# Kernel tuning notes

Hardware: AMD Instinct MI355X
Metric: run time of the kernel (lower is better)

The kernel has to match this reference:

```python
import jax, jax.numpy as jnp
import numpy as np

N = 50000          # nodes
E = 625000         # edges
H = 128            # hidden_dim
L = 4              # num_layers
G = 2000           # number of graphs in batch
NODE_F = 9
EDGE_F = 4
LN_EPS = 1e-5


def setup_inputs() -> dict:
    key = jax.random.key(0)
    ks = jax.random.split(key, 14)
    s = 0.05
    return {
        "x": jax.random.normal(ks[0], (N, NODE_F), jnp.float32),
        "edge_index": jax.random.randint(ks[1], (2, E), 0, N, dtype=jnp.int32),
        "edge_attr": jax.random.normal(ks[2], (E, EDGE_F), jnp.float32),
        "batch": jnp.sort(jax.random.randint(ks[3], (N,), 0, G, dtype=jnp.int32)),
        # node / edge encoders
        "Wn": jax.random.normal(ks[4], (NODE_F, H), jnp.float32) * s,
        "bn": jnp.zeros((H,), jnp.float32),
        "We": jax.random.normal(ks[5], (EDGE_F, H), jnp.float32) * s,
        "be": jnp.zeros((H,), jnp.float32),
        # per-layer GINE MLP params (stacked over layers)
        "W1": jax.random.normal(ks[6], (L, H, 2 * H), jnp.float32) * s,
        "b1": jnp.zeros((L, 2 * H), jnp.float32),
        "W2": jax.random.normal(ks[7], (L, 2 * H, H), jnp.float32) * s,
        "b2": jnp.zeros((L, H), jnp.float32),
        # per-layer LayerNorm params
        "gamma": jnp.ones((L, H), jnp.float32),
        "beta": jnp.zeros((L, H), jnp.float32),
    }


def reference(x, edge_index, edge_attr, batch, Wn, bn, We, be, W1, b1, W2, b2, gamma, beta):
    h = x @ Wn + bn                       # [N, H]
    ea = edge_attr @ We + be              # [E, H]
    src, dst = edge_index[0], edge_index[1]
    for l in range(L):
        res = h
        # GINEConv (eps=0): out = mlp(x + sum_j relu(x_j + e_ij))
        msg = jax.nn.relu(h[src] + ea)                              # [E, H] gather+add+relu
        agg = jax.ops.segment_sum(msg, dst, num_segments=N)        # scatter-sum -> [N, H]
        z = h + agg
        z = jax.nn.relu(z @ W1[l] + b1[l]) @ W2[l] + b2[l]          # 2-layer MLP
        mu = jnp.mean(z, axis=-1, keepdims=True)
        var = jnp.mean((z - mu) ** 2, axis=-1, keepdims=True)
        z = (z - mu) * jax.lax.rsqrt(var + LN_EPS) * gamma[l] + beta[l]
        h = jax.nn.relu(z) + res                                    # relu + residual
    # global_add_pool
    return jax.ops.segment_sum(h, batch, num_segments=G)            # [G, H]
```

## Files before the change

### kernel.cpp

```cpp
#include <hip/hip_runtime.h>

typedef unsigned short ushort_t;
typedef __attribute__((ext_vector_type(8))) __bf16 bf16x8;
typedef __attribute__((ext_vector_type(4))) float f32x4;

#define HD 128
#define NL 4
#define SCAN_C 2048

__device__ __forceinline__ ushort_t f2bf(float f){
  unsigned u = __builtin_bit_cast(unsigned, f);
  unsigned r = (u + 0x7FFFu + ((u >> 16) & 1u)) >> 16;
  return (ushort_t)r;
}

__device__ __forceinline__ float bf2f(ushort_t u){
  unsigned v = ((unsigned)u) << 16;
  return __builtin_bit_cast(float, v);
}

__device__ __forceinline__ f32x4 mfma16(bf16x8 a, bf16x8 b, f32x4 c){
  return __builtin_amdgcn_mfma_f32_16x16x32_bf16(a, b, c, 0, 0, 0);
}

__global__ void hist_kernel(const int* __restrict__ dst, int* __restrict__ deg, int E){
  int e = blockIdx.x * 256 + threadIdx.x;
  if (e < E) atomicAdd(&deg[dst[e]], 1);
}

__global__ void ghist_kernel(const int* __restrict__ batch, int* __restrict__ gdeg, int N){
  int n = blockIdx.x * 256 + threadIdx.x;
  if (n < N) atomicAdd(&gdeg[batch[n]], 1);
}

__global__ void scan_part(const int* __restrict__ in, int* __restrict__ bsum, int n){
  int b = blockIdx.x, tid = threadIdx.x;
  int base = b * SCAN_C + tid * 8;
  int s = 0;
  if (base + 8 <= n){
    int4 a = *(const int4*)(in + base);
    int4 c = *(const int4*)(in + base + 4);
    s = a.x + a.y + a.z + a.w + c.x + c.y + c.z + c.w;
  } else {
    #pragma unroll
    for (int k = 0; k < 8; ++k) if (base + k < n) s += in[base + k];
  }
  #pragma unroll
  for (int o = 1; o < 64; o <<= 1) s += __shfl_xor(s, o, 64);
  __shared__ int ws[4];
  int lane = tid & 63, wid = tid >> 6;
  if (lane == 0) ws[wid] = s;
  __syncthreads();
  if (tid == 0) bsum[b] = ws[0] + ws[1] + ws[2] + ws[3];
}

__global__ void scan_top(const int* __restrict__ bsum, int* __restrict__ bofs,
                         int* __restrict__ outn, int B){
  int tid = threadIdx.x;
  int v = (tid < B) ? bsum[tid] : 0;
  int lane = tid & 63, wid = tid >> 6;
  int inc = v;
  #pragma unroll
  for (int o = 1; o < 64; o <<= 1){
    int t = __shfl_up(inc, o, 64);
    if (lane >= o) inc += t;
  }
  __shared__ int ws[4];
  if (lane == 63) ws[wid] = inc;
  __syncthreads();
  int wprev = 0;
  for (int i = 0; i < wid; ++i) wprev += ws[i];
  if (tid < B) bofs[tid] = inc - v + wprev;
  if (tid == 0) *outn = ws[0] + ws[1] + ws[2] + ws[3];
}

__global__ void scan_final(const int* __restrict__ in, const int* __restrict__ bofs,
                           int* __restrict__ out, int* __restrict__ cur, int n){
  int b = blockIdx.x, tid = threadIdx.x;
  int base = b * SCAN_C + tid * 8;
  int v[8];
  if (base + 8 <= n){
    *(int4*)(v)     = *(const int4*)(in + base);
    *(int4*)(v + 4) = *(const int4*)(in + base + 4);
  } else {
    #pragma unroll
    for (int k = 0; k < 8; ++k) v[k] = (base + k < n) ? in[base + k] : 0;
  }
  int tsum = 0;
  #pragma unroll
  for (int k = 0; k < 8; ++k) tsum += v[k];
  int lane = tid & 63, wid = tid >> 6;
  int inc = tsum;
  #pragma unroll
  for (int o = 1; o < 64; o <<= 1){
    int t = __shfl_up(inc, o, 64);
    if (lane >= o) inc += t;
  }
  __shared__ int ws[4];
  if (lane == 63) ws[wid] = inc;
  __syncthreads();
  int run = bofs[b] + inc - tsum;
  for (int i = 0; i < wid; ++i) run += ws[i];
  #pragma unroll
  for (int k = 0; k < 8; ++k){
    int i = base + k;
    if (i < n){
      out[i] = run;
      if (cur) cur[i] = run;
      run += v[k];
    }
  }
}

__global__ void scatter_kernel(const int* __restrict__ src, const int* __restrict__ dst,
                               const float4* __restrict__ ea, int* __restrict__ cursor,
                               int* __restrict__ srcs_s, float4* __restrict__ ea4_s, int E){
  int e = blockIdx.x * 256 + threadIdx.x;
  if (e < E){
    int d = dst[e];
    int p = atomicAdd(&cursor[d], 1);
    srcs_s[p] = src[e];
    ea4_s[p] = ea[e];
  }
}

__global__ void wconv_kernel(const float* __restrict__ W1, const float* __restrict__ W2,
                             ushort_t* __restrict__ W1t, ushort_t* __restrict__ W2t){
  int i = blockIdx.x * 256 + threadIdx.x;
  if (i < NL * 32768){
    int l = i >> 15, r = i & 32767;
    int n = r >> 7, k = r & 127;
    W1t[i] = f2bf(W1[l * 32768 + k * 256 + n]);
  } else {
    int i2 = i - NL * 32768;
    int l = i2 >> 15, r = i2 & 32767;
    int n = r >> 8, k = r & 255;
    W2t[i2] = f2bf(W2[l * 32768 + k * 128 + n]);
  }
}

__global__ void encoder_kernel(const float* __restrict__ x, const float* __restrict__ Wn,
                               const float* __restrict__ bn, float* __restrict__ h,
                               ushort_t* __restrict__ hb, int N){
  int n = blockIdx.x, j = threadIdx.x;
  float acc = bn[j];
  #pragma unroll
  for (int k = 0; k < 9; ++k) acc = fmaf(x[n * 9 + k], Wn[k * HD + j], acc);
  h[(size_t)n * HD + j] = acc;
  hb[(size_t)n * HD + j] = f2bf(acc);
}

__global__ void agg_kernel(const float* __restrict__ h, const ushort_t* __restrict__ hb,
                           const int* __restrict__ off, const int* __restrict__ srcs,
                           const float4* __restrict__ ea4, const float* __restrict__ We,
                           const float* __restrict__ be, ushort_t* __restrict__ z, int N){
  int n = blockIdx.x, j = threadIdx.x;
  float w0 = We[j], w1 = We[HD + j], w2 = We[2 * HD + j], w3 = We[3 * HD + j];
  float bj = be[j];
  int s = off[n], e = off[n + 1];
  float acc = h[(size_t)n * HD + j];
  int i = s;
  for (; i + 4 <= e; i += 4){
    int s0 = srcs[i], s1 = srcs[i + 1], s2 = srcs[i + 2], s3 = srcs[i + 3];
    float4 a0 = ea4[i], a1 = ea4[i + 1], a2 = ea4[i + 2], a3 = ea4[i + 3];
    float h0 = bf2f(hb[(size_t)s0 * HD + j]);
    float h1 = bf2f(hb[(size_t)s1 * HD + j]);
    float h2 = bf2f(hb[(size_t)s2 * HD + j]);
    float h3 = bf2f(hb[(size_t)s3 * HD + j]);
    float e0 = fmaf(a0.x, w0, fmaf(a0.y, w1, fmaf(a0.z, w2, fmaf(a0.w, w3, bj))));
    float e1 = fmaf(a1.x, w0, fmaf(a1.y, w1, fmaf(a1.z, w2, fmaf(a1.w, w3, bj))));
    float e2 = fmaf(a2.x, w0, fmaf(a2.y, w1, fmaf(a2.z, w2, fmaf(a2.w, w3, bj))));
    float e3 = fmaf(a3.x, w0, fmaf(a3.y, w1, fmaf(a3.z, w2, fmaf(a3.w, w3, bj))));
    acc += fmaxf(h0 + e0, 0.f);
    acc += fmaxf(h1 + e1, 0.f);
    acc += fmaxf(h2 + e2, 0.f);
    acc += fmaxf(h3 + e3, 0.f);
  }
  for (; i < e; ++i){
    int sc = srcs[i];
    float4 a = ea4[i];
    float eav = fmaf(a.x, w0, fmaf(a.y, w1, fmaf(a.z, w2, fmaf(a.w, w3, bj))));
    acc += fmaxf(bf2f(hb[(size_t)sc * HD + j]) + eav, 0.f);
  }
  z[(size_t)n * HD + j] = f2bf(acc);
}

__global__ __launch_bounds__(256, 2) void mlp1_kernel(
    const ushort_t* __restrict__ z, const ushort_t* __restrict__ Bt,
    const float* __restrict__ bias, ushort_t* __restrict__ outp, int N){
  extern __shared__ char smem[];
  char* As = smem;
  char* Bs = smem + 32768;
  int tid = threadIdx.x;
  int r0 = blockIdx.x * 128;
  int c0 = blockIdx.y * 128;
  #pragma unroll
  for (int i = 0; i < 8; ++i){
    int g = i * 256 + tid;
    int row = g >> 4, kg = g & 15;
    int lb = row * 256 + ((kg * 16) ^ ((row & 7) << 4));
    int ar = min(r0 + row, N - 1);
    *(bf16x8*)(As + lb) = *(const bf16x8*)(z + (size_t)ar * 128 + kg * 8);
    *(bf16x8*)(Bs + lb) = *(const bf16x8*)(Bt + (size_t)(c0 + row) * 128 + kg * 8);
  }
  __syncthreads();
  int w = tid >> 6, l = tid & 63;
  int wr = w >> 1, wc = w & 1;
  int lr = l & 15, lk = l >> 4;
  f32x4 acc[4][4] = {};
  #pragma unroll
  for (int ks = 0; ks < 4; ++ks){
    int kb = ks * 64 + lk * 16;
    bf16x8 a[4], b[4];
    #pragma unroll
    for (int fm = 0; fm < 4; ++fm){
      int row = wr * 64 + fm * 16 + lr;
      a[fm] = *(const bf16x8*)(As + row * 256 + (kb ^ ((row & 7) << 4)));
    }
    #pragma unroll
    for (int fn = 0; fn < 4; ++fn){
      int col = wc * 64 + fn * 16 + lr;
      b[fn] = *(const bf16x8*)(Bs + col * 256 + (kb ^ ((col & 7) << 4)));
    }
    #pragma unroll
    for (int fm = 0; fm < 4; ++fm)
      #pragma unroll
      for (int fn = 0; fn < 4; ++fn)
        acc[fm][fn] = mfma16(a[fm], b[fn], acc[fm][fn]);
  }
  float bv[4];
  #pragma unroll
  for (int fn = 0; fn < 4; ++fn) bv[fn] = bias[c0 + wc * 64 + fn * 16 + lr];
  #pragma unroll
  for (int fm = 0; fm < 4; ++fm){
    #pragma unroll
    for (int r = 0; r < 4; ++r){
      int row = r0 + wr * 64 + fm * 16 + lk * 4 + r;
      if (row < N){
        #pragma unroll
        for (int fn = 0; fn < 4; ++fn){
          int col = c0 + wc * 64 + fn * 16 + lr;
          outp[(size_t)row * 256 + col] = f2bf(fmaxf(acc[fm][fn][r] + bv[fn], 0.f));
        }
      }
    }
  }
}

__global__ __launch_bounds__(256, 2) void mlp2_kernel(
    const ushort_t* __restrict__ tin, const ushort_t* __restrict__ Bt,
    const float* __restrict__ b2, const float* __restrict__ gamma,
    const float* __restrict__ beta, float* __restrict__ h,
    ushort_t* __restrict__ hb, int N){
  extern __shared__ char smem[];
  char* As = smem;
  char* Bs = smem + 32768;
  float* z2 = (float*)smem;
  float* stat = (float*)(smem + 66560);
  int tid = threadIdx.x;
  int r0 = blockIdx.x * 128;
  int w = tid >> 6, l = tid & 63;
  int wr = w >> 1, wc = w & 1;
  int lr = l & 15, lk = l >> 4;
  f32x4 acc[4][4] = {};
  for (int kh = 0; kh < 2; ++kh){
    #pragma unroll
    for (int i = 0; i < 8; ++i){
      int g = i * 256 + tid;
      int row = g >> 4, kg = g & 15;
      int lb = row * 256 + ((kg * 16) ^ ((row & 7) << 4));
      int ar = min(r0 + row, N - 1);
      *(bf16x8*)(As + lb) = *(const bf16x8*)(tin + (size_t)ar * 256 + kh * 128 + kg * 8);
      *(bf16x8*)(Bs + lb) = *(const bf16x8*)(Bt + (size_t)row * 256 + kh * 128 + kg * 8);
    }
    __syncthreads();
    #pragma unroll
    for (int ks = 0; ks < 4; ++ks){
      int kb = ks * 64 + lk * 16;
      bf16x8 a[4], b[4];
      #pragma unroll
      for (int fm = 0; fm < 4; ++fm){
        int row = wr * 64 + fm * 16 + lr;
        a[fm] = *(const bf16x8*)(As + row * 256 + (kb ^ ((row & 7) << 4)));
      }
      #pragma unroll
      for (int fn = 0; fn < 4; ++fn){
        int col = wc * 64 + fn * 16 + lr;
        b[fn] = *(const bf16x8*)(Bs + col * 256 + (kb ^ ((col & 7) << 4)));
      }
      #pragma unroll
      for (int fm = 0; fm < 4; ++fm)
        #pragma unroll
        for (int fn = 0; fn < 4; ++fn)
          acc[fm][fn] = mfma16(a[fm], b[fn], acc[fm][fn]);
    }
    __syncthreads();
  }
  float bv[4];
  #pragma unroll
  for (int fn = 0; fn < 4; ++fn) bv[fn] = b2[wc * 64 + fn * 16 + lr];
  #pragma unroll
  for (int fm = 0; fm < 4; ++fm)
    #pragma unroll
    for (int r = 0; r < 4; ++r){
      int row = wr * 64 + fm * 16 + lk * 4 + r;
      #pragma unroll
      for (int fn = 0; fn < 4; ++fn){
        int col = wc * 64 + fn * 16 + lr;
        z2[row * 130 + col] = acc[fm][fn][r] + bv[fn];
      }
    }
  __syncthreads();
  {
    int row = tid >> 1, hf = tid & 1;
    const float* q = z2 + row * 130 + hf * 64;
    float s = 0.f, qq = 0.f;
    #pragma unroll
    for (int i = 0; i < 32; ++i){
      float2 v = *(const float2*)(q + i * 2);
      s += v.x + v.y; qq += v.x * v.x + v.y * v.y;
    }
    s += __shfl_xor(s, 1, 64);
    qq += __shfl_xor(qq, 1, 64);
    if (hf == 0){
      float mean = s * (1.f / 128.f);
      float var = qq * (1.f / 128.f) - mean * mean;
      stat[row] = mean;
      stat[128 + row] = rsqrtf(var + 1e-5f);
    }
  }
  __syncthreads();
  #pragma unroll 4
  for (int it = 0; it < 32; ++it){
    int row = it * 4 + (tid >> 6);
    int grow = r0 + row;
    if (grow < N){
      int col = (tid & 63) * 2;
      float2 v = *(const float2*)(z2 + row * 130 + col);
      float m = stat[row], rs = stat[128 + row];
      float2 g = *(const float2*)(gamma + col);
      float2 bt = *(const float2*)(beta + col);
      float2 hr = *(const float2*)(h + (size_t)grow * HD + col);
      float2 ov;
      ov.x = fmaxf((v.x - m) * rs * g.x + bt.x, 0.f) + hr.x;
      ov.y = fmaxf((v.y - m) * rs * g.y + bt.y, 0.f) + hr.y;
      *(float2*)(h + (size_t)grow * HD + col) = ov;
      ushort_t b0 = f2bf(ov.x), b1v = f2bf(ov.y);
      *(unsigned*)(hb + (size_t)grow * HD + col) = (unsigned)b0 | ((unsigned)b1v << 16);
    }
  }
}

__global__ void pool_kernel(const float* __restrict__ h, const int* __restrict__ goff,
                            float* __restrict__ outp, int G){
  int g = blockIdx.x, j = threadIdx.x;
  int s = goff[g], e = goff[g + 1];
  float acc = 0.f;
  for (int i = s; i < e; ++i) acc += h[(size_t)i * HD + j];
  outp[(size_t)g * HD + j] = acc;
}

extern "C" void kernel_launch(void* const* d_in, const int* in_sizes, int n_in,
                              void* d_out, int out_size, void* d_ws, size_t ws_size,
                              hipStream_t stream){
  const float* x     = (const float*)d_in[0];
  const int*   ei    = (const int*)  d_in[1];
  const float* eattr = (const float*)d_in[2];
  const int*   batch = (const int*)  d_in[3];
  const float* Wn    = (const float*)d_in[4];
  const float* bn    = (const float*)d_in[5];
  const float* We    = (const float*)d_in[6];
  const float* be    = (const float*)d_in[7];
  const float* W1    = (const float*)d_in[8];
  const float* b1    = (const float*)d_in[9];
  const float* W2    = (const float*)d_in[10];
  const float* b2    = (const float*)d_in[11];
  const float* gamma = (const float*)d_in[12];
  const float* beta  = (const float*)d_in[13];
  float* outp = (float*)d_out;

  int N = in_sizes[3];
  int E = in_sizes[2] / 4;
  int G = out_size / HD;

  char* base = (char*)d_ws;
  size_t o = 0;
  auto alloc = [&](size_t bytes)->char*{
    char* r = base + o; o = (o + bytes + 255) & ~(size_t)255; return r;
  };
  float*    h    = (float*)   alloc((size_t)N * HD * 4);
  ushort_t* hb   = (ushort_t*)alloc((size_t)N * HD * 2);
  ushort_t* z    = (ushort_t*)alloc((size_t)N * HD * 2);
  ushort_t* t    = (ushort_t*)alloc((size_t)N * 2 * HD * 2);
  ushort_t* W1t  = (ushort_t*)alloc((size_t)NL * 2 * HD * HD * 2);
  ushort_t* W2t  = (ushort_t*)alloc((size_t)NL * 2 * HD * HD * 2);
  int* deg    = (int*)alloc((size_t)N * 4);
  int* gdeg   = (int*)alloc((size_t)G * 4);
  int* off    = (int*)alloc((size_t)(N + 1) * 4);
  int* goff   = (int*)alloc((size_t)(G + 1) * 4);
  int* cursor = (int*)alloc((size_t)N * 4);
  int* bsumN  = (int*)alloc(512 * 4);
  int* bofsN  = (int*)alloc(512 * 4);
  int* bsumG  = (int*)alloc(512 * 4);
  int* bofsG  = (int*)alloc(512 * 4);
  int* srcs_s = (int*)alloc((size_t)E * 4);
  float4* ea4 = (float4*)alloc((size_t)E * 16);
  (void)ws_size; (void)n_in;

  const int* src = ei;
  const int* dst = ei + E;

  hipMemsetAsync(deg, 0, (size_t)N * 4, stream);
  hipMemsetAsync(gdeg, 0, (size_t)G * 4, stream);

  hist_kernel<<<(E + 255) / 256, 256, 0, stream>>>(dst, deg, E);
  ghist_kernel<<<(N + 255) / 256, 256, 0, stream>>>(batch, gdeg, N);

  int BN = (N + SCAN_C - 1) / SCAN_C;
  int BG = (G + SCAN_C - 1) / SCAN_C;
  scan_part<<<BN, 256, 0, stream>>>(deg, bsumN, N);
  scan_top<<<1, 256, 0, stream>>>(bsumN, bofsN, off + N, BN);
  scan_final<<<BN, 256, 0, stream>>>(deg, bofsN, off, cursor, N);
  scan_part<<<BG, 256, 0, stream>>>(gdeg, bsumG, G);
  scan_top<<<1, 256, 0, stream>>>(bsumG, bofsG, goff + G, BG);
  scan_final<<<BG, 256, 0, stream>>>(gdeg, bofsG, goff, (int*)nullptr, G);

  scatter_kernel<<<(E + 255) / 256, 256, 0, stream>>>(src, dst, (const float4*)eattr,
                                                      cursor, srcs_s, ea4, E);
  wconv_kernel<<<(2 * NL * 32768) / 256, 256, 0, stream>>>(W1, W2, W1t, W2t);
  encoder_kernel<<<N, HD, 0, stream>>>(x, Wn, bn, h, hb, N);

  int mblocks = (N + 127) / 128;
  for (int l = 0; l < NL; ++l){
    agg_kernel<<<N, HD, 0, stream>>>(h, hb, off, srcs_s, ea4, We, be, z, N);
    mlp1_kernel<<<dim3(mblocks, 2), 256, 65536, stream>>>(
        z, W1t + (size_t)l * 2 * HD * HD, b1 + l * 2 * HD, t, N);
    mlp2_kernel<<<mblocks, 256, 67584, stream>>>(
        t, W2t + (size_t)l * 2 * HD * HD, b2 + l * HD, gamma + l * HD, beta + l * HD, h, hb, N);
  }
  pool_kernel<<<G, HD, 0, stream>>>(h, goff, outp, G);
}
```

Measured before the change: 447.0 us.

## Fuse GINE MLP layers into one kernel and index edge attrs indirectly

```diff
diff --git a/kernel.cpp b/kernel.cpp
--- a/kernel.cpp
+++ b/kernel.cpp
@@ -113,14 +113,12 @@
 }
 
 __global__ void scatter_kernel(const int* __restrict__ src, const int* __restrict__ dst,
-                               const float4* __restrict__ ea, int* __restrict__ cursor,
-                               int* __restrict__ srcs_s, float4* __restrict__ ea4_s, int E){
+                               int* __restrict__ cursor, int2* __restrict__ se, int E){
   int e = blockIdx.x * 256 + threadIdx.x;
   if (e < E){
     int d = dst[e];
     int p = atomicAdd(&cursor[d], 1);
-    srcs_s[p] = src[e];
-    ea4_s[p] = ea[e];
+    se[p] = make_int2(src[e], e);
   }
 }
 
@@ -151,7 +149,7 @@
 }
 
 __global__ void agg_kernel(const float* __restrict__ h, const ushort_t* __restrict__ hb,
-                           const int* __restrict__ off, const int* __restrict__ srcs,
+                           const int* __restrict__ off, const int2* __restrict__ se,
                            const float4* __restrict__ ea4, const float* __restrict__ We,
                            const float* __restrict__ be, ushort_t* __restrict__ z, int N){
   int n = blockIdx.x, j = threadIdx.x;
@@ -161,12 +159,12 @@
   float acc = h[(size_t)n * HD + j];
   int i = s;
   for (; i + 4 <= e; i += 4){
-    int s0 = srcs[i], s1 = srcs[i + 1], s2 = srcs[i + 2], s3 = srcs[i + 3];
-    float4 a0 = ea4[i], a1 = ea4[i + 1], a2 = ea4[i + 2], a3 = ea4[i + 3];
-    float h0 = bf2f(hb[(size_t)s0 * HD + j]);
-    float h1 = bf2f(hb[(size_t)s1 * HD + j]);
-    float h2 = bf2f(hb[(size_t)s2 * HD + j]);
-    float h3 = bf2f(hb[(size_t)s3 * HD + j]);
+    int2 p0 = se[i], p1 = se[i + 1], p2 = se[i + 2], p3 = se[i + 3];
+    float4 a0 = ea4[p0.y], a1 = ea4[p1.y], a2 = ea4[p2.y], a3 = ea4[p3.y];
+    float h0 = bf2f(hb[(size_t)p0.x * HD + j]);
+    float h1 = bf2f(hb[(size_t)p1.x * HD + j]);
+    float h2 = bf2f(hb[(size_t)p2.x * HD + j]);
+    float h3 = bf2f(hb[(size_t)p3.x * HD + j]);
     float e0 = fmaf(a0.x, w0, fmaf(a0.y, w1, fmaf(a0.z, w2, fmaf(a0.w, w3, bj))));
     float e1 = fmaf(a1.x, w0, fmaf(a1.y, w1, fmaf(a1.z, w2, fmaf(a1.w, w3, bj))));
     float e2 = fmaf(a2.x, w0, fmaf(a2.y, w1, fmaf(a2.z, w2, fmaf(a2.w, w3, bj))));
@@ -177,176 +175,152 @@
     acc += fmaxf(h3 + e3, 0.f);
   }
   for (; i < e; ++i){
-    int sc = srcs[i];
-    float4 a = ea4[i];
+    int2 p = se[i];
+    float4 a = ea4[p.y];
     float eav = fmaf(a.x, w0, fmaf(a.y, w1, fmaf(a.z, w2, fmaf(a.w, w3, bj))));
-    acc += fmaxf(bf2f(hb[(size_t)sc * HD + j]) + eav, 0.f);
+    acc += fmaxf(bf2f(hb[(size_t)p.x * HD + j]) + eav, 0.f);
   }
   z[(size_t)n * HD + j] = f2bf(acc);
 }
 
-__global__ __launch_bounds__(256, 2) void mlp1_kernel(
-    const ushort_t* __restrict__ z, const ushort_t* __restrict__ Bt,
-    const float* __restrict__ bias, ushort_t* __restrict__ outp, int N){
-  extern __shared__ char smem[];
-  char* As = smem;
-  char* Bs = smem + 32768;
+__global__ __launch_bounds__(512, 4) void mlp_fused_kernel(
+    const ushort_t* __restrict__ zin, const ushort_t* __restrict__ W1t,
+    const float* __restrict__ b1, const ushort_t* __restrict__ W2t,
+    const float* __restrict__ b2, const float* __restrict__ gamma,
+    const float* __restrict__ beta, float* __restrict__ h,
+    ushort_t* __restrict__ hb, int N){
+  extern __shared__ char lds[];
   int tid = threadIdx.x;
   int r0 = blockIdx.x * 128;
-  int c0 = blockIdx.y * 128;
-  #pragma unroll
-  for (int i = 0; i < 8; ++i){
-    int g = i * 256 + tid;
+  #pragma unroll
+  for (int i = 0; i < 4; ++i){
+    int g = i * 512 + tid;
     int row = g >> 4, kg = g & 15;
     int lb = row * 256 + ((kg * 16) ^ ((row & 7) << 4));
     int ar = min(r0 + row, N - 1);
-    *(bf16x8*)(As + lb) = *(const bf16x8*)(z + (size_t)ar * 128 + kg * 8);
-    *(bf16x8*)(Bs + lb) = *(const bf16x8*)(Bt + (size_t)(c0 + row) * 128 + kg * 8);
-  }
-  __syncthreads();
+    *(bf16x8*)(lds + lb) = *(const bf16x8*)(zin + (size_t)ar * 128 + kg * 8);
+  }
   int w = tid >> 6, l = tid & 63;
-  int wr = w >> 1, wc = w & 1;
   int lr = l & 15, lk = l >> 4;
-  f32x4 acc[4][4] = {};
-  #pragma unroll
-  for (int ks = 0; ks < 4; ++ks){
-    int kb = ks * 64 + lk * 16;
-    bf16x8 a[4], b[4];
-    #pragma unroll
-    for (int fm = 0; fm < 4; ++fm){
-      int row = wr * 64 + fm * 16 + lr;
-      a[fm] = *(const bf16x8*)(As + row * 256 + (kb ^ ((row & 7) << 4)));
-    }
-    #pragma unroll
-    for (int fn = 0; fn < 4; ++fn){
-      int col = wc * 64 + fn * 16 + lr;
-      b[fn] = *(const bf16x8*)(Bs + col * 256 + (kb ^ ((col & 7) << 4)));
-    }
-    #pragma unroll
-    for (int fm = 0; fm < 4; ++fm)
-      #pragma unroll
-      for (int fn = 0; fn < 4; ++fn)
-        acc[fm][fn] = mfma16(a[fm], b[fn], acc[fm][fn]);
-  }
-  float bv[4];
-  #pragma unroll
-  for (int fn = 0; fn < 4; ++fn) bv[fn] = bias[c0 + wc * 64 + fn * 16 + lr];
-  #pragma unroll
-  for (int fm = 0; fm < 4; ++fm){
-    #pragma unroll
-    for (int r = 0; r < 4; ++r){
-      int row = r0 + wr * 64 + fm * 16 + lk * 4 + r;
-      if (row < N){
-        #pragma unroll
-        for (int fn = 0; fn < 4; ++fn){
-          int col = c0 + wc * 64 + fn * 16 + lr;
-          outp[(size_t)row * 256 + col] = f2bf(fmaxf(acc[fm][fn][r] + bv[fn], 0.f));
-        }
-      }
-    }
-  }
-}
-
-__global__ __launch_bounds__(256, 2) void mlp2_kernel(
-    const ushort_t* __restrict__ tin, const ushort_t* __restrict__ Bt,
-    const float* __restrict__ b2, const float* __restrict__ gamma,
-    const float* __restrict__ beta, float* __restrict__ h,
-    ushort_t* __restrict__ hb, int N){
-  extern __shared__ char smem[];
-  char* As = smem;
-  char* Bs = smem + 32768;
-  float* z2 = (float*)smem;
-  float* stat = (float*)(smem + 66560);
-  int tid = threadIdx.x;
-  int r0 = blockIdx.x * 128;
-  int w = tid >> 6, l = tid & 63;
-  int wr = w >> 1, wc = w & 1;
-  int lr = l & 15, lk = l >> 4;
-  f32x4 acc[4][4] = {};
-  for (int kh = 0; kh < 2; ++kh){
-    #pragma unroll
-    for (int i = 0; i < 8; ++i){
-      int g = i * 256 + tid;
-      int row = g >> 4, kg = g & 15;
-      int lb = row * 256 + ((kg * 16) ^ ((row & 7) << 4));
-      int ar = min(r0 + row, N - 1);
-      *(bf16x8*)(As + lb) = *(const bf16x8*)(tin + (size_t)ar * 256 + kh * 128 + kg * 8);
-      *(bf16x8*)(Bs + lb) = *(const bf16x8*)(Bt + (size_t)row * 256 + kh * 128 + kg * 8);
-    }
-    __syncthreads();
+  __syncthreads();
+  {
+    int wk = w >> 1, wn = w & 1;
+    f32x4 acc1[4][4] = {};
     #pragma unroll
     for (int ks = 0; ks < 4; ++ks){
       int kb = ks * 64 + lk * 16;
       bf16x8 a[4], b[4];
       #pragma unroll
       for (int fm = 0; fm < 4; ++fm){
-        int row = wr * 64 + fm * 16 + lr;
-        a[fm] = *(const bf16x8*)(As + row * 256 + (kb ^ ((row & 7) << 4)));
+        int k2r = wk * 64 + fm * 16 + lr;
+        a[fm] = *(const bf16x8*)((const char*)W1t + (size_t)k2r * 256 + kb);
       }
       #pragma unroll
       for (int fn = 0; fn < 4; ++fn){
-        int col = wc * 64 + fn * 16 + lr;
-        b[fn] = *(const bf16x8*)(Bs + col * 256 + (kb ^ ((col & 7) << 4)));
+        int node = wn * 64 + fn * 16 + lr;
+        b[fn] = *(const bf16x8*)(lds + node * 256 + (kb ^ ((node & 7) << 4)));
       }
       #pragma unroll
       for (int fm = 0; fm < 4; ++fm)
         #pragma unroll
         for (int fn = 0; fn < 4; ++fn)
-          acc[fm][fn] = mfma16(a[fm], b[fn], acc[fm][fn]);
+          acc1[fm][fn] = mfma16(a[fm], b[fn], acc1[fm][fn]);
     }
     __syncthreads();
-  }
-  float bv[4];
-  #pragma unroll
-  for (int fn = 0; fn < 4; ++fn) bv[fn] = b2[wc * 64 + fn * 16 + lr];
-  #pragma unroll
-  for (int fm = 0; fm < 4; ++fm)
-    #pragma unroll
-    for (int r = 0; r < 4; ++r){
-      int row = wr * 64 + fm * 16 + lk * 4 + r;
+    #pragma unroll
+    for (int fm = 0; fm < 4; ++fm){
+      f32x4 bv = *(const f32x4*)(b1 + wk * 64 + fm * 16 + lk * 4);
+      int k2b = (wk * 64 + fm * 16 + lk * 4) * 2;
       #pragma unroll
       for (int fn = 0; fn < 4; ++fn){
-        int col = wc * 64 + fn * 16 + lr;
-        z2[row * 130 + col] = acc[fm][fn][r] + bv[fn];
+        int node = wn * 64 + fn * 16 + lr;
+        ushort4 tv;
+        tv.x = f2bf(fmaxf(acc1[fm][fn][0] + bv[0], 0.f));
+        tv.y = f2bf(fmaxf(acc1[fm][fn][1] + bv[1], 0.f));
+        tv.z = f2bf(fmaxf(acc1[fm][fn][2] + bv[2], 0.f));
+        tv.w = f2bf(fmaxf(acc1[fm][fn][3] + bv[3], 0.f));
+        *(ushort4*)(lds + node * 512 + (k2b ^ ((node & 7) << 4))) = tv;
       }
     }
-  __syncthreads();
-  {
-    int row = tid >> 1, hf = tid & 1;
-    const float* q = z2 + row * 130 + hf * 64;
-    float s = 0.f, qq = 0.f;
-    #pragma unroll
-    for (int i = 0; i < 32; ++i){
-      float2 v = *(const float2*)(q + i * 2);
-      s += v.x + v.y; qq += v.x * v.x + v.y * v.y;
-    }
-    s += __shfl_xor(s, 1, 64);
-    qq += __shfl_xor(qq, 1, 64);
-    if (hf == 0){
-      float mean = s * (1.f / 128.f);
-      float var = qq * (1.f / 128.f) - mean * mean;
-      stat[row] = mean;
-      stat[128 + row] = rsqrtf(var + 1e-5f);
-    }
-  }
-  __syncthreads();
-  #pragma unroll 4
-  for (int it = 0; it < 32; ++it){
-    int row = it * 4 + (tid >> 6);
-    int grow = r0 + row;
-    if (grow < N){
-      int col = (tid & 63) * 2;
-      float2 v = *(const float2*)(z2 + row * 130 + col);
-      float m = stat[row], rs = stat[128 + row];
-      float2 g = *(const float2*)(gamma + col);
-      float2 bt = *(const float2*)(beta + col);
-      float2 hr = *(const float2*)(h + (size_t)grow * HD + col);
-      float2 ov;
-      ov.x = fmaxf((v.x - m) * rs * g.x + bt.x, 0.f) + hr.x;
-      ov.y = fmaxf((v.y - m) * rs * g.y + bt.y, 0.f) + hr.y;
-      *(float2*)(h + (size_t)grow * HD + col) = ov;
-      ushort_t b0 = f2bf(ov.x), b1v = f2bf(ov.y);
-      *(unsigned*)(hb + (size_t)grow * HD + col) = (unsigned)b0 | ((unsigned)b1v << 16);
+  }
+  __syncthreads();
+  int wd = w >> 1, wn2 = w & 1;
+  f32x4 acc2[2][4] = {};
+  #pragma unroll
+  for (int ks = 0; ks < 8; ++ks){
+    int kb = ks * 64 + lk * 16;
+    bf16x8 a2[2], bt2[4];
+    #pragma unroll
+    for (int fm = 0; fm < 2; ++fm){
+      int d = wd * 32 + fm * 16 + lr;
+      a2[fm] = *(const bf16x8*)((const char*)W2t + (size_t)d * 512 + kb);
+    }
+    #pragma unroll
+    for (int fn = 0; fn < 4; ++fn){
+      int node = wn2 * 64 + fn * 16 + lr;
+      bt2[fn] = *(const bf16x8*)(lds + node * 512 + (kb ^ ((node & 7) << 4)));
+    }
+    #pragma unroll
+    for (int fm = 0; fm < 2; ++fm)
+      #pragma unroll
+      for (int fn = 0; fn < 4; ++fn)
+        acc2[fm][fn] = mfma16(a2[fm], bt2[fn], acc2[fm][fn]);
+  }
+  __syncthreads();
+  float* stat_s = (float*)lds;
+  float* stat_q = (float*)(lds + 2048);
+  f32x4 b2v[2], gv[2], btv[2];
+  #pragma unroll
+  for (int fm = 0; fm < 2; ++fm){
+    int db = wd * 32 + fm * 16 + lk * 4;
+    b2v[fm] = *(const f32x4*)(b2 + db);
+    gv[fm]  = *(const f32x4*)(gamma + db);
+    btv[fm] = *(const f32x4*)(beta + db);
+  }
+  #pragma unroll
+  for (int fn = 0; fn < 4; ++fn){
+    float ss = 0.f, qq = 0.f;
+    #pragma unroll
+    for (int fm = 0; fm < 2; ++fm)
+      #pragma unroll
+      for (int r = 0; r < 4; ++r){
+        float v = acc2[fm][fn][r] + b2v[fm][r];
+        acc2[fm][fn][r] = v;
+        ss += v; qq += v * v;
+      }
+    ss += __shfl_xor(ss, 16, 64); ss += __shfl_xor(ss, 32, 64);
+    qq += __shfl_xor(qq, 16, 64); qq += __shfl_xor(qq, 32, 64);
+    if (l < 16){
+      int node = wn2 * 64 + fn * 16 + lr;
+      stat_s[node * 4 + wd] = ss;
+      stat_q[node * 4 + wd] = qq;
+    }
+  }
+  __syncthreads();
+  #pragma unroll
+  for (int fn = 0; fn < 4; ++fn){
+    int node = wn2 * 64 + fn * 16 + lr;
+    int gn = r0 + node;
+    float ss = stat_s[node * 4 + 0] + stat_s[node * 4 + 1] +
+               stat_s[node * 4 + 2] + stat_s[node * 4 + 3];
+    float qq = stat_q[node * 4 + 0] + stat_q[node * 4 + 1] +
+               stat_q[node * 4 + 2] + stat_q[node * 4 + 3];
+    float mean = ss * (1.f / 128.f);
+    float rs = rsqrtf(qq * (1.f / 128.f) - mean * mean + 1e-5f);
+    if (gn < N){
+      #pragma unroll
+      for (int fm = 0; fm < 2; ++fm){
+        int db = wd * 32 + fm * 16 + lk * 4;
+        f32x4 hold = *(const f32x4*)(h + (size_t)gn * HD + db);
+        f32x4 ov;
+        #pragma unroll
+        for (int r = 0; r < 4; ++r)
+          ov[r] = fmaxf((acc2[fm][fn][r] - mean) * rs * gv[fm][r] + btv[fm][r], 0.f) + hold[r];
+        *(f32x4*)(h + (size_t)gn * HD + db) = ov;
+        ushort4 hv;
+        hv.x = f2bf(ov[0]); hv.y = f2bf(ov[1]); hv.z = f2bf(ov[2]); hv.w = f2bf(ov[3]);
+        *(ushort4*)(hb + (size_t)gn * HD + db) = hv;
+      }
     }
   }
 }
@@ -391,7 +365,6 @@
   float*    h    = (float*)   alloc((size_t)N * HD * 4);
   ushort_t* hb   = (ushort_t*)alloc((size_t)N * HD * 2);
   ushort_t* z    = (ushort_t*)alloc((size_t)N * HD * 2);
-  ushort_t* t    = (ushort_t*)alloc((size_t)N * 2 * HD * 2);
   ushort_t* W1t  = (ushort_t*)alloc((size_t)NL * 2 * HD * HD * 2);
   ushort_t* W2t  = (ushort_t*)alloc((size_t)NL * 2 * HD * HD * 2);
   int* deg    = (int*)alloc((size_t)N * 4);
@@ -403,8 +376,7 @@
   int* bofsN  = (int*)alloc(512 * 4);
   int* bsumG  = (int*)alloc(512 * 4);
   int* bofsG  = (int*)alloc(512 * 4);
-  int* srcs_s = (int*)alloc((size_t)E * 4);
-  float4* ea4 = (float4*)alloc((size_t)E * 16);
+  int2* se    = (int2*)alloc((size_t)E * 8);
   (void)ws_size; (void)n_in;
 
   const int* src = ei;
@@ -425,18 +397,17 @@
   scan_top<<<1, 256, 0, stream>>>(bsumG, bofsG, goff + G, BG);
   scan_final<<<BG, 256, 0, stream>>>(gdeg, bofsG, goff, (int*)nullptr, G);
 
-  scatter_kernel<<<(E + 255) / 256, 256, 0, stream>>>(src, dst, (const float4*)eattr,
-                                                      cursor, srcs_s, ea4, E);
+  scatter_kernel<<<(E + 255) / 256, 256, 0, stream>>>(src, dst, cursor, se, E);
   wconv_kernel<<<(2 * NL * 32768) / 256, 256, 0, stream>>>(W1, W2, W1t, W2t);
   encoder_kernel<<<N, HD, 0, stream>>>(x, Wn, bn, h, hb, N);
 
   int mblocks = (N + 127) / 128;
   for (int l = 0; l < NL; ++l){
-    agg_kernel<<<N, HD, 0, stream>>>(h, hb, off, srcs_s, ea4, We, be, z, N);
-    mlp1_kernel<<<dim3(mblocks, 2), 256, 65536, stream>>>(
-        z, W1t + (size_t)l * 2 * HD * HD, b1 + l * 2 * HD, t, N);
-    mlp2_kernel<<<mblocks, 256, 67584, stream>>>(
-        t, W2t + (size_t)l * 2 * HD * HD, b2 + l * HD, gamma + l * HD, beta + l * HD, h, hb, N);
+    agg_kernel<<<N, HD, 0, stream>>>(h, hb, off, se, (const float4*)eattr, We, be, z, N);
+    mlp_fused_kernel<<<mblocks, 512, 65536, stream>>>(
+        z, W1t + (size_t)l * 2 * HD * HD, b1 + l * 2 * HD,
+        W2t + (size_t)l * 2 * HD * HD, b2 + l * HD,
+        gamma + l * HD, beta + l * HD, h, hb, N);
   }
   pool_kernel<<<G, HD, 0, stream>>>(h, goff, outp, G);
 }
```

Measured after the change: 479.9 us. 1.07x slower.
